# Performance work log

Hardware: AMD Instinct MI355X
Metric: run time of the kernel (lower is better)

## Reference

```python
import jax, jax.numpy as jnp
import numpy as np
from jax import lax

NUM_LAYERS, C, HIDDEN = 3, 64, 128
B, H, W = 16, 128, 128
DC = C // 4  # partial-conv channels (dim_conv = dim // 4)


def _conv2d(x, w, b=None, groups=1):
    # x: [B,C,H,W], w: [O, C//groups, kh, kw], SAME padding, stride 1
    y = lax.conv_general_dilated(x, w, (1, 1), 'SAME',
                                 dimension_numbers=('NCHW', 'OIHW', 'NCHW'),
                                 feature_group_count=groups)
    return y if b is None else y + b[None, :, None, None]


def _pw(x, w, b):
    # 1x1x1 Conv3d at T=1 == pointwise channel mix. w: [O, C], b: [O]
    return jnp.einsum('oc,bchw->bohw', w, x) + b[None, :, None, None]


def _gelu(x):
    return jax.nn.gelu(x, approximate=False)  # torch nn.GELU default (erf)


def setup_inputs() -> dict:
    key = jax.random.key(0)
    ks = jax.random.split(key, 18)
    s = 0.1
    return {
        'x': jax.random.normal(ks[0], (B, C, H, W), jnp.float32),
        'wz1': jax.random.normal(ks[1], (NUM_LAYERS, C, C), jnp.float32) * s,
        'bz1': jax.random.normal(ks[2], (NUM_LAYERS, C), jnp.float32) * s,
        'wz2': jax.random.normal(ks[3], (NUM_LAYERS, C, C), jnp.float32) * s,
        'bz2': jax.random.normal(ks[4], (NUM_LAYERS, C), jnp.float32) * s,
        'wf1': jax.random.normal(ks[5], (NUM_LAYERS, C, C), jnp.float32) * s,
        'bf1': jax.random.normal(ks[6], (NUM_LAYERS, C), jnp.float32) * s,
        'wf2': jax.random.normal(ks[7], (NUM_LAYERS, C, C), jnp.float32) * s,
        'bf2': jax.random.normal(ks[8], (NUM_LAYERS, C), jnp.float32) * s,
        # FRFN
        'pconv_w': jax.random.normal(ks[9], (NUM_LAYERS, DC, DC, 3, 3), jnp.float32) * s,
        'lin1_w': jax.random.normal(ks[10], (NUM_LAYERS, C, 2 * HIDDEN), jnp.float32) * s,
        'lin1_b': jax.random.normal(ks[11], (NUM_LAYERS, 2 * HIDDEN), jnp.float32) * s,
        'dw_w': jax.random.normal(ks[12], (NUM_LAYERS, HIDDEN, 1, 3, 3), jnp.float32) * s,
        'dw_b': jax.random.normal(ks[13], (NUM_LAYERS, HIDDEN), jnp.float32) * s,
        'lin2_w': jax.random.normal(ks[14], (NUM_LAYERS, HIDDEN, C), jnp.float32) * s,
        'lin2_b': jax.random.normal(ks[15], (NUM_LAYERS, C), jnp.float32) * s,
        # conv_out: in_dim -> out_dim=1, 3x3
        'out_w': jax.random.normal(ks[16], (1, C, 3, 3), jnp.float32) * s,
        'out_b': jax.random.normal(ks[17], (1,), jnp.float32) * s,
    }


def reference(x, wz1, bz1, wz2, bz2, wf1, bf1, wf2, bf2,
              pconv_w, lin1_w, lin1_b, dw_w, dw_b, lin2_w, lin2_b,
              out_w, out_b):
    x_init = x
    for l in range(NUM_LAYERS):
        # ---- MHRB: time dim is 1 (x.unsqueeze(2)), so flips over dim 2 are
        # identities and the recurrence is a single step h = (1 - F) * Z.
        Z = jnp.tanh(_pw(jnp.tanh(_pw(x, wz1[l], bz1[l])), wz2[l], bz2[l]))
        F = jax.nn.sigmoid(_pw(jnp.tanh(_pw(x, wf1[l], bf1[l])), wf2[l], bf2[l]))
        x = (1.0 - F) * Z
        # ---- FRFN (operates on b (h w) c; equivalently on NCHW channel dim)
        res = x
        x1 = _conv2d(x[:, :DC], pconv_w[l])            # partial 3x3 conv, no bias
        x = jnp.concatenate([x1, x[:, DC:]], axis=1)
        h = _gelu(jnp.einsum('bchw,ck->bkhw', x, lin1_w[l])
                  + lin1_b[l][None, :, None, None])    # linear1 + GELU
        h1, h2 = h[:, :HIDDEN], h[:, HIDDEN:]          # chunk(2, dim=-1)
        h1 = _gelu(_conv2d(h1, dw_w[l], dw_b[l], groups=HIDDEN))  # dwconv + GELU
        g = h1 * h2                                    # gating
        x = (jnp.einsum('bkhw,kc->bchw', g, lin2_w[l])
             + lin2_b[l][None, :, None, None]) + res   # linear2 + residual
    return _conv2d(x + x_init, out_w, out_b)           # conv_out
```

## Files before the change

kernel.cpp:

```cpp
#include <hip/hip_runtime.h>
#include <hip/hip_bf16.h>

#define CC 64
#define HIDN 128
#define DCC 16
#define HH 128
#define WW 128
#define HWS (HH*WW)
#define BB 16
#define NPIX (BB*HWS)

typedef __hip_bfloat16 bf16;
typedef __attribute__((ext_vector_type(8))) unsigned short ushort8;
typedef __attribute__((ext_vector_type(4))) unsigned short ushort4v;
typedef __attribute__((ext_vector_type(4))) float float4v;
typedef __attribute__((ext_vector_type(8))) short bf16x8;
typedef __attribute__((ext_vector_type(4))) float f32x4;

__device__ __forceinline__ float rcp_fast(float x){ return __builtin_amdgcn_rcpf(x); }
__device__ __forceinline__ float ftanh(float x){
    float e = __expf(2.f*x);
    return 1.f - 2.f*rcp_fast(e + 1.f);
}
__device__ __forceinline__ float fsig(float x){
    return rcp_fast(1.f + __expf(-x));
}
__device__ __forceinline__ float fgelu(float x){
    return x * fsig(x*(1.5957691216f + 0.07135481283f*x*x));
}
__device__ __forceinline__ float b2f(bf16 v){ return __bfloat162float(v); }
__device__ __forceinline__ float u2f(unsigned short u){
    unsigned v = ((unsigned)u) << 16; return __uint_as_float(v);
}
__device__ __forceinline__ unsigned short f2u(float f){
    bf16 h = __float2bfloat16(f);
    return *reinterpret_cast<unsigned short*>(&h);
}
__device__ __forceinline__ bf16x8 packf(float4v a, float4v b){
    bf16x8 r;
    r[0]=(short)f2u(a.x); r[1]=(short)f2u(a.y); r[2]=(short)f2u(a.z); r[3]=(short)f2u(a.w);
    r[4]=(short)f2u(b.x); r[5]=(short)f2u(b.y); r[6]=(short)f2u(b.z); r[7]=(short)f2u(b.w);
    return r;
}

template<int F32>
__global__ __launch_bounds__(256,2) void k_gate(
    const float* __restrict__ xf, const bf16* __restrict__ xb,
    const float* __restrict__ wz1, const float* __restrict__ bz1,
    const float* __restrict__ wz2, const float* __restrict__ bz2,
    const float* __restrict__ wf1, const float* __restrict__ bf1,
    const float* __restrict__ wf2, const float* __restrict__ bf2,
    bf16* __restrict__ vout)
{
    __shared__ __align__(16) unsigned short xs[512*64];
    const int t = threadIdx.x;
    const int lane = t & 63;
    const int wv = t >> 6;
    const int col = lane & 15;
    const int g = lane >> 4;
    const int blk = blockIdx.x;
    const int b = blk >> 5;
    const int sp0 = (blk & 31) << 9;

    {
        const int ch = t & 63;
        const int wg = t >> 6;
        const size_t base = ((size_t)b*CC + ch)*HWS + sp0;
        #pragma unroll
        for (int i=0;i<16;++i){
            int bufpx = (wg*16 + i) << 3;
            ushort8 val;
            if (F32){
                float4v a = *reinterpret_cast<const float4v*>(xf + base + bufpx);
                float4v c = *reinterpret_cast<const float4v*>(xf + base + bufpx + 4);
                val[0]=f2u(a.x); val[1]=f2u(a.y); val[2]=f2u(a.z); val[3]=f2u(a.w);
                val[4]=f2u(c.x); val[5]=f2u(c.y); val[6]=f2u(c.z); val[7]=f2u(c.w);
            } else {
                val = *reinterpret_cast<const ushort8*>(xb + base + bufpx);
            }
            #pragma unroll
            for (int j=0;j<8;++j){
                int px = bufpx + j;
                *(unsigned short*)((char*)xs + px*128 + ((ch*2) ^ ((px&7)<<4))) = val[j];
            }
        }
    }

    bf16x8 Az1[4][2], Af1[4][2], Az2[4][2], Af2[4][2];
    #pragma unroll
    for (int ot=0; ot<4; ++ot){
        #pragma unroll
        for (int kh=0; kh<2; ++kh){
            const float* p;
            p = wz1 + (ot*16+col)*64 + kh*32 + g*8;
            Az1[ot][kh] = packf(*(const float4v*)p, *(const float4v*)(p+4));
            p = wf1 + (ot*16+col)*64 + kh*32 + g*8;
            Af1[ot][kh] = packf(*(const float4v*)p, *(const float4v*)(p+4));
            p = wz2 + (ot*16+col)*64 + kh*32 + g*4;
            Az2[ot][kh] = packf(*(const float4v*)p, *(const float4v*)(p+16));
            p = wf2 + (ot*16+col)*64 + kh*32 + g*4;
            Af2[ot][kh] = packf(*(const float4v*)p, *(const float4v*)(p+16));
        }
    }
    __syncthreads();

    bf16* vb = vout + (size_t)b*CC*HWS;

    for (int it = wv; it < 32; it += 4){
        const int lpx = it*16 + col;
        const int px = sp0 + lpx;
        bf16x8 Bx[2];
        Bx[0] = *(const bf16x8*)((char*)xs + lpx*128 + ((g*16) ^ ((lpx&7)<<4)));
        Bx[1] = *(const bf16x8*)((char*)xs + lpx*128 + ((64 + g*16) ^ ((lpx&7)<<4)));
        f32x4 Dz[4], Df[4];
        #pragma unroll
        for (int ot=0; ot<4; ++ot){
            Dz[ot] = *(const f32x4*)(bz1 + ot*16 + g*4);
            Df[ot] = *(const f32x4*)(bf1 + ot*16 + g*4);
        }
        #pragma unroll
        for (int kh=0; kh<2; ++kh)
            #pragma unroll
            for (int ot=0; ot<4; ++ot){
                Dz[ot] = __builtin_amdgcn_mfma_f32_16x16x32_bf16(Az1[ot][kh], Bx[kh], Dz[ot], 0,0,0);
                Df[ot] = __builtin_amdgcn_mfma_f32_16x16x32_bf16(Af1[ot][kh], Bx[kh], Df[ot], 0,0,0);
            }
        #pragma unroll
        for (int ot=0; ot<4; ++ot)
            #pragma unroll
            for (int r=0; r<4; ++r){
                Dz[ot][r] = ftanh(Dz[ot][r]);
                Df[ot][r] = ftanh(Df[ot][r]);
            }
        bf16x8 Bz[2], Bf[2];
        #pragma unroll
        for (int kh=0; kh<2; ++kh)
            #pragma unroll
            for (int j=0; j<4; ++j){
                Bz[kh][j]   = (short)f2u(Dz[2*kh][j]);
                Bz[kh][4+j] = (short)f2u(Dz[2*kh+1][j]);
                Bf[kh][j]   = (short)f2u(Df[2*kh][j]);
                Bf[kh][4+j] = (short)f2u(Df[2*kh+1][j]);
            }
        f32x4 Ez[4], Ef[4];
        #pragma unroll
        for (int ot=0; ot<4; ++ot){
            Ez[ot] = *(const f32x4*)(bz2 + ot*16 + g*4);
            Ef[ot] = *(const f32x4*)(bf2 + ot*16 + g*4);
        }
        #pragma unroll
        for (int kh=0; kh<2; ++kh)
            #pragma unroll
            for (int ot=0; ot<4; ++ot){
                Ez[ot] = __builtin_amdgcn_mfma_f32_16x16x32_bf16(Az2[ot][kh], Bz[kh], Ez[ot], 0,0,0);
                Ef[ot] = __builtin_amdgcn_mfma_f32_16x16x32_bf16(Af2[ot][kh], Bf[kh], Ef[ot], 0,0,0);
            }
        #pragma unroll
        for (int ot=0; ot<4; ++ot)
            #pragma unroll
            for (int r=0; r<4; ++r){
                float Zv = ftanh(Ez[ot][r]);
                float Fv = fsig(Ef[ot][r]);
                *reinterpret_cast<unsigned short*>(vb + (size_t)(ot*16+g*4+r)*HWS + px)
                    = f2u((1.f - Fv)*Zv);
            }
    }
}

__global__ __launch_bounds__(256) void k_pconv(
    const bf16* __restrict__ v, const float* __restrict__ w, bf16* __restrict__ x1)
{
    int blk0 = blockIdx.x;
    int blk = (blk0 & 7)*32 + (blk0 >> 3);
    int gid = blk*256 + threadIdx.x;
    int b = gid >> 12;
    int sp4 = (gid & 4095) << 2;
    int y = sp4 >> 7, x0 = sp4 & 127;
    const bf16* vb = v + (size_t)b*CC*HWS;
    float acc[DCC][4];
    #pragma unroll
    for (int o=0;o<DCC;++o)
        #pragma unroll
        for (int i=0;i<4;++i) acc[o][i] = 0.f;

    #pragma unroll 1
    for (int ic=0; ic<DCC; ++ic){
        const bf16* ip = vb + (size_t)ic*HWS;
        float xv[3][6];
        #pragma unroll
        for (int ky=0;ky<3;++ky){
            int yy = y + ky - 1;
            if (yy >= 0 && yy < HH){
                const bf16* rp = ip + yy*WW + x0;
                ushort4v mv = *reinterpret_cast<const ushort4v*>(rp);
                xv[ky][1]=u2f(mv[0]); xv[ky][2]=u2f(mv[1]);
                xv[ky][3]=u2f(mv[2]); xv[ky][4]=u2f(mv[3]);
                xv[ky][0] = (x0>0)     ? b2f(rp[-1]) : 0.f;
                xv[ky][5] = (x0+4<WW)  ? b2f(rp[4])  : 0.f;
            } else {
                #pragma unroll
                for (int i=0;i<6;++i) xv[ky][i] = 0.f;
            }
        }
        #pragma unroll
        for (int o=0;o<DCC;++o){
            const float* wp = w + (size_t)(o*DCC+ic)*9;
            #pragma unroll
            for (int ky=0;ky<3;++ky){
                float w0 = wp[ky*3+0], w1 = wp[ky*3+1], w2 = wp[ky*3+2];
                #pragma unroll
                for (int i=0;i<4;++i)
                    acc[o][i] = fmaf(w0, xv[ky][i],
                                fmaf(w1, xv[ky][i+1],
                                fmaf(w2, xv[ky][i+2], acc[o][i])));
            }
        }
    }
    bf16* xo = x1 + (size_t)b*DCC*HWS + sp4;
    #pragma unroll
    for (int o=0;o<DCC;++o){
        ushort4v ov;
        #pragma unroll
        for (int i=0;i<4;++i) ov[i] = f2u(acc[o][i]);
        *reinterpret_cast<ushort4v*>(xo + (size_t)o*HWS) = ov;
    }
}

__global__ __launch_bounds__(256) void k_lin1h(
    const bf16* __restrict__ x1, const bf16* __restrict__ v,
    const float* __restrict__ l1w, const float* __restrict__ l1b,
    bf16* __restrict__ h1out)
{
    __shared__ __align__(16) unsigned short xs[256*64];
    __shared__ __align__(16) unsigned short tr[4][32*66];
    const int t = threadIdx.x;
    const int lane = t & 63;
    const int wv = t >> 6;
    const int col = lane & 15;
    const int g = lane >> 4;
    const int blk = blockIdx.x;
    const int b = blk >> 6;
    const int sp0 = (blk & 63) << 8;

    {
        const int ch = t & 63;
        const int wg = t >> 6;
        const bf16* src = (ch < DCC) ? x1 + ((size_t)b*DCC + ch)*HWS
                                     : v  + ((size_t)b*CC  + ch)*HWS;
        #pragma unroll
        for (int i=0;i<8;++i){
            int bufpx = (wg*8 + i) << 3;
            ushort8 val = *reinterpret_cast<const ushort8*>(src + sp0 + bufpx);
            #pragma unroll
            for (int j=0;j<8;++j){
                int px = bufpx + j;
                *(unsigned short*)((char*)xs + px*128 + ((ch*2) ^ ((px&7)<<4))) = val[j];
            }
        }
    }
    __syncthreads();

    unsigned short* trw = &tr[wv][0];
    const int lpx0 = wv*64;

    #pragma unroll 1
    for (int oc=0; oc<4; ++oc){
        bf16x8 A1[2][2];
        #pragma unroll
        for (int t2=0;t2<2;++t2)
            #pragma unroll
            for (int kh=0;kh<2;++kh){
                bf16x8 fa;
                #pragma unroll
                for (int j=0;j<8;++j){
                    int cin = kh*32 + g*8 + j;
                    fa[j] = (short)f2u(l1w[cin*256 + oc*32 + t2*16 + col]);
                }
                A1[t2][kh]=fa;
            }
        #pragma unroll
        for (int lt=0;lt<4;++lt){
            int px = lpx0 + lt*16 + col;
            bf16x8 B0 = *(const bf16x8*)((char*)xs + px*128 + ((g*16) ^ ((px&7)<<4)));
            bf16x8 B1 = *(const bf16x8*)((char*)xs + px*128 + ((64 + g*16) ^ ((px&7)<<4)));
            f32x4 D0 = *(const f32x4*)(l1b + oc*32 + g*4);
            f32x4 D1 = *(const f32x4*)(l1b + oc*32 + 16 + g*4);
            D0 = __builtin_amdgcn_mfma_f32_16x16x32_bf16(A1[0][0], B0, D0, 0,0,0);
            D0 = __builtin_amdgcn_mfma_f32_16x16x32_bf16(A1[0][1], B1, D0, 0,0,0);
            D1 = __builtin_amdgcn_mfma_f32_16x16x32_bf16(A1[1][0], B0, D1, 0,0,0);
            D1 = __builtin_amdgcn_mfma_f32_16x16x32_bf16(A1[1][1], B1, D1, 0,0,0);
            int lp = lt*16 + col;
            #pragma unroll
            for (int rr=0;rr<4;++rr){
                trw[(g*4+rr)*66 + lp]    = f2u(fgelu(D0[rr]));
                trw[(16+g*4+rr)*66 + lp] = f2u(fgelu(D1[rr]));
            }
        }
        {
            int ch2 = lane >> 1;
            int half = lane & 1;
            const unsigned short* srcp = trw + ch2*66 + half*32;
            bf16* dst = h1out + ((size_t)(b*HIDN + oc*32 + ch2))*HWS + sp0 + lpx0 + half*32;
            #pragma unroll
            for (int i=0;i<4;++i){
                ushort8 u8 = *reinterpret_cast<const ushort8*>(srcp + i*8);
                *reinterpret_cast<ushort8*>(dst + i*8) = u8;
            }
        }
    }
}

__global__ __launch_bounds__(256) void k_wprep(
    const float* __restrict__ l1w_all, const float* __restrict__ w2_all,
    bf16* __restrict__ frag_all)
{
    const int l = blockIdx.x;
    const float* l1w = l1w_all + (size_t)l*CC*256;
    const float* w2  = w2_all  + (size_t)l*HIDN*CC;
    unsigned short* buf1 = (unsigned short*)(frag_all + (size_t)l*16384);
    unsigned short* buf2 = buf1 + 8192;
    const int t = threadIdx.x;
    const int lane = t & 63;
    const int col = lane & 15;
    const int g = lane >> 4;
    #pragma unroll
    for (int c4=0;c4<4;++c4){
        int combo = (t>>6)*4 + c4;
        {
            int cc = combo >> 2, t2 = (combo>>1)&1, kh = combo&1;
            #pragma unroll
            for (int j=0;j<8;++j){
                int cin = kh*32 + g*8 + j;
                buf1[(combo*64 + lane)*8 + j] =
                    f2u(l1w[cin*256 + 128 + cc*32 + t2*16 + col]);
            }
        }
        {
            int cc = combo >> 2, ot = combo & 3;
            #pragma unroll
            for (int j=0;j<8;++j){
                int k = cc*32 + ((j>>2)<<4) + (g<<2) + (j&3);
                buf2[(combo*64 + lane)*8 + j] = f2u(w2[k*64 + ot*16 + col]);
            }
        }
    }
}

__global__ __launch_bounds__(256) void k_dwA(
    const bf16* __restrict__ x1, const bf16* __restrict__ v,
    const bf16* __restrict__ h1, const bf16* __restrict__ wfrag,
    const float* __restrict__ l1b,
    const float* __restrict__ dww, const float* __restrict__ dwb,
    const float* __restrict__ l2b,
    bf16* __restrict__ xout,
    const float* __restrict__ xinit,
    bf16* __restrict__ xsum)
{
    __shared__ __align__(16) unsigned short xs[128*64];
    __shared__ __align__(16) unsigned short ubuf[2*8320];
    const int t = threadIdx.x;
    const int lane = t & 63;
    const int wv = t >> 6;
    const int col = lane & 15;
    const int g = lane >> 4;
    const int blk0 = blockIdx.x;
    const int blk = (blk0 & 7)*256 + (blk0 >> 3);
    const int b = blk >> 7;
    const int y = blk & 127;

    const int cj  = (t>>3) & 31;
    const int pxo = (t & 7) << 4;

    const unsigned short* buf1 = (const unsigned short*)wfrag;
    const unsigned short* buf2 = buf1 + 8192;

    ushort8 pfa[3], pfb[3];
    unsigned short pfl[3], pfr[3];
    float pw9[9], pbj;
    auto LOADCHUNK = [&](int cc){
        int chg = cc*32 + cj;
        const bf16* h1p = h1 + ((size_t)(b*HIDN + chg))*HWS;
        #pragma unroll
        for (int ky=0; ky<3; ++ky){
            int gy = y + ky - 1;
            if (gy >= 0 && gy < HH){
                const bf16* rp = h1p + (size_t)gy*WW + pxo;
                pfa[ky] = *reinterpret_cast<const ushort8*>(rp);
                pfb[ky] = *reinterpret_cast<const ushort8*>(rp+8);
                pfl[ky] = (pxo>0)     ? *reinterpret_cast<const unsigned short*>(rp-1)  : 0;
                pfr[ky] = (pxo+16<WW) ? *reinterpret_cast<const unsigned short*>(rp+16) : 0;
            } else {
                #pragma unroll
                for (int i=0;i<8;++i){ pfa[ky][i]=0; pfb[ky][i]=0; }
                pfl[ky]=0; pfr[ky]=0;
            }
        }
        #pragma unroll
        for (int i=0;i<9;++i) pw9[i] = dww[chg*9+i];
        pbj = dwb[chg];
    };

    LOADCHUNK(0);

    {
        const int ch = t & 63;
        const int wg = t >> 6;
        const bf16* src = (ch < DCC) ? x1 + ((size_t)b*DCC + ch)*HWS
                                     : v  + ((size_t)b*CC  + ch)*HWS;
        #pragma unroll
        for (int i=0;i<2;++i){
            int bufpx = (wg*2 + i) << 3;
            ushort8 val = *reinterpret_cast<const ushort8*>(src + (size_t)y*WW + bufpx);
            #pragma unroll
            for (int j=0;j<8;++j){
                int px = bufpx + j;
                *(unsigned short*)((char*)xs + px*128 + ((ch*2) ^ ((px&7)<<4))) = val[j];
            }
        }
    }
    __syncthreads();

    f32x4 Dx[2][4];
    #pragma unroll
    for (int q=0;q<2;++q)
        #pragma unroll
        for (int ot=0;ot<4;++ot)
            Dx[q][ot] = *(const f32x4*)(l2b + ot*16 + g*4);

    #pragma unroll 1
    for (int cc=0; cc<4; ++cc){
        unsigned short* ub = ubuf + (cc&1)*8320;
        ushort8 o0v, o1v;
        {
            float acc[16];
            #pragma unroll
            for (int i=0;i<16;++i) acc[i]=0.f;
            #pragma unroll
            for (int ky=0; ky<3; ++ky){
                float m[16];
                #pragma unroll
                for (int i=0;i<8;++i){ m[i]=u2f(pfa[ky][i]); m[8+i]=u2f(pfb[ky][i]); }
                float lf = u2f(pfl[ky]);
                float rt = u2f(pfr[ky]);
                float w0=pw9[ky*3], w1=pw9[ky*3+1], wv2=pw9[ky*3+2];
                #pragma unroll
                for (int i=0;i<16;++i){
                    float l  = i ? m[i-1] : lf;
                    float r_ = (i==15) ? rt : m[i+1];
                    acc[i] = fmaf(w0,l, fmaf(w1,m[i], fmaf(wv2,r_,acc[i])));
                }
            }
            #pragma unroll
            for (int i=0;i<8;++i){
                o0v[i] = f2u(fgelu(acc[i]+pbj));
                o1v[i] = f2u(fgelu(acc[8+i]+pbj));
            }
        }
        if (cc < 3) LOADCHUNK(cc+1);
        *(ushort8*)(ub + cj*260 + pxo)     = o0v;
        *(ushort8*)(ub + cj*260 + pxo + 8) = o1v;
        __syncthreads();
        {
            bf16x8 A1g[2][2];
            #pragma unroll
            for (int t2=0;t2<2;++t2)
                #pragma unroll
                for (int kh=0;kh<2;++kh){
                    int combo = (cc*2+t2)*2+kh;
                    ushort8 u = *reinterpret_cast<const ushort8*>(buf1 + (combo*64 + lane)*8);
                    bf16x8 f;
                    #pragma unroll
                    for (int j=0;j<8;++j) f[j]=(short)u[j];
                    A1g[t2][kh]=f;
                }
            bf16x8 A2[4];
            #pragma unroll
            for (int ot=0;ot<4;++ot){
                int combo = cc*4+ot;
                ushort8 u = *reinterpret_cast<const ushort8*>(buf2 + (combo*64 + lane)*8);
                bf16x8 f;
                #pragma unroll
                for (int j=0;j<8;++j) f[j]=(short)u[j];
                A2[ot] = f;
            }
            #pragma unroll
            for (int q=0;q<2;++q){
                int px = (wv*2+q)*16 + col;
                bf16x8 B0 = *(const bf16x8*)((char*)xs + px*128 + ((g*16) ^ ((px&7)<<4)));
                bf16x8 B1 = *(const bf16x8*)((char*)xs + px*128 + ((64 + g*16) ^ ((px&7)<<4)));
                f32x4 D0 = *(const f32x4*)(l1b + 128 + cc*32 + g*4);
                f32x4 D1 = *(const f32x4*)(l1b + 128 + cc*32 + 16 + g*4);
                D0 = __builtin_amdgcn_mfma_f32_16x16x32_bf16(A1g[0][0], B0, D0, 0,0,0);
                D0 = __builtin_amdgcn_mfma_f32_16x16x32_bf16(A1g[0][1], B1, D0, 0,0,0);
                D1 = __builtin_amdgcn_mfma_f32_16x16x32_bf16(A1g[1][0], B0, D1, 0,0,0);
                D1 = __builtin_amdgcn_mfma_f32_16x16x32_bf16(A1g[1][1], B1, D1, 0,0,0);
                bf16x8 Bg;
                #pragma unroll
                for (int j=0;j<4;++j){
                    float u0 = u2f(ub[(g*4+j)*260 + px]);
                    float u1 = u2f(ub[(16+g*4+j)*260 + px]);
                    Bg[j]   = (short)f2u(u0 * fgelu(D0[j]));
                    Bg[4+j] = (short)f2u(u1 * fgelu(D1[j]));
                }
                #pragma unroll
                for (int ot=0;ot<4;++ot)
                    Dx[q][ot] = __builtin_amdgcn_mfma_f32_16x16x32_bf16(A2[ot], Bg, Dx[q][ot], 0,0,0);
            }
        }
    }
    __syncthreads();
    #pragma unroll
    for (int q=0;q<2;++q)
        #pragma unroll
        for (int ot=0;ot<4;++ot)
            #pragma unroll
            for (int rr=0;rr<4;++rr)
                ubuf[(ot*16 + g*4 + rr)*136 + (wv*2+q)*16 + col] = f2u(Dx[q][ot][rr]);
    __syncthreads();
    {
        int ch  = t >> 2;
        int pxb = (t & 3) * 32;
        size_t off = ((size_t)(b*CC + ch))*HWS + (size_t)y*WW + pxb;
        #pragma unroll
        for (int i=0;i<4;++i){
            ushort8 dv = *reinterpret_cast<const ushort8*>(ubuf + ch*136 + pxb + i*8);
            ushort8 vv = *reinterpret_cast<const ushort8*>(v + off + i*8);
            ushort8 ov;
            float rv[8];
            #pragma unroll
            for (int j=0;j<8;++j){
                rv[j] = u2f(dv[j]) + u2f(vv[j]);
                ov[j] = f2u(rv[j]);
            }
            *reinterpret_cast<ushort8*>(xout + off + i*8) = ov;
            if (xinit){
                float4v x0 = *reinterpret_cast<const float4v*>(xinit + off + i*8);
                float4v x1v = *reinterpret_cast<const float4v*>(xinit + off + i*8 + 4);
                ushort8 sv;
                sv[0]=f2u(rv[0]+x0.x); sv[1]=f2u(rv[1]+x0.y);
                sv[2]=f2u(rv[2]+x0.z); sv[3]=f2u(rv[3]+x0.w);
                sv[4]=f2u(rv[4]+x1v.x); sv[5]=f2u(rv[5]+x1v.y);
                sv[6]=f2u(rv[6]+x1v.z); sv[7]=f2u(rv[7]+x1v.w);
                *reinterpret_cast<ushort8*>(xsum + off + i*8) = sv;
            }
        }
    }
}

__global__ __launch_bounds__(256) void k_final(
    const bf16* __restrict__ s, const float* __restrict__ w,
    const float* __restrict__ bias, float* __restrict__ out)
{
    int gid = blockIdx.x*256 + threadIdx.x;
    int b = gid >> 12;
    int sp4 = (gid & 4095) << 2;
    int y = sp4 >> 7, x0 = sp4 & 127;
    const bf16* sb = s + (size_t)b*CC*HWS;
    float acc[4];
    #pragma unroll
    for (int i=0;i<4;++i) acc[i] = bias[0];

    #pragma unroll 1
    for (int c=0;c<CC;++c){
        const bf16* ip = sb + (size_t)c*HWS;
        const float* wp = w + (size_t)c*9;
        #pragma unroll
        for (int ky=0;ky<3;++ky){
            int yy = y + ky - 1;
            float xv[6];
            if (yy >= 0 && yy < HH){
                const bf16* rp = ip + yy*WW + x0;
                ushort4v mv = *reinterpret_cast<const ushort4v*>(rp);
                xv[1]=u2f(mv[0]); xv[2]=u2f(mv[1]); xv[3]=u2f(mv[2]); xv[4]=u2f(mv[3]);
                xv[0] = (x0>0)    ? b2f(rp[-1]) : 0.f;
                xv[5] = (x0+4<WW) ? b2f(rp[4])  : 0.f;
            } else {
                #pragma unroll
                for (int i=0;i<6;++i) xv[i] = 0.f;
            }
            float w0 = wp[ky*3+0], w1 = wp[ky*3+1], w2 = wp[ky*3+2];
            #pragma unroll
            for (int i=0;i<4;++i)
                acc[i] = fmaf(w0, xv[i],
                         fmaf(w1, xv[i+1],
                         fmaf(w2, xv[i+2], acc[i])));
        }
    }
    float4v ov; ov.x=acc[0]; ov.y=acc[1]; ov.z=acc[2]; ov.w=acc[3];
    *reinterpret_cast<float4v*>(out + (size_t)gid*4) = ov;
}

extern "C" void kernel_launch(void* const* d_in, const int* in_sizes, int n_in,
                              void* d_out, int out_size, void* d_ws, size_t ws_size,
                              hipStream_t stream)
{
    const float* x    = (const float*)d_in[0];
    const float* wz1  = (const float*)d_in[1];
    const float* bz1  = (const float*)d_in[2];
    const float* wz2  = (const float*)d_in[3];
    const float* bz2  = (const float*)d_in[4];
    const float* wf1  = (const float*)d_in[5];
    const float* bf1  = (const float*)d_in[6];
    const float* wf2  = (const float*)d_in[7];
    const float* bf2  = (const float*)d_in[8];
    const float* pw   = (const float*)d_in[9];
    const float* l1w  = (const float*)d_in[10];
    const float* l1b  = (const float*)d_in[11];
    const float* dww  = (const float*)d_in[12];
    const float* dwb  = (const float*)d_in[13];
    const float* l2w  = (const float*)d_in[14];
    const float* l2b  = (const float*)d_in[15];
    const float* ow   = (const float*)d_in[16];
    const float* obb  = (const float*)d_in[17];

    char* ws = (char*)d_ws;
    bf16* xc    = (bf16*)(ws);
    bf16* v     = (bf16*)(ws + 33554432);
    bf16* x1    = (bf16*)(ws + 67108864);
    bf16* xsumb = (bf16*)(ws + 75497472);
    bf16* h1buf = (bf16*)(ws + 109051904);
    bf16* wfrag = (bf16*)(ws + 176160768);

    k_wprep<<<3, 256, 0, stream>>>(l1w, l2w, wfrag);
    for (int l=0;l<3;++l){
        if (l == 0)
            k_gate<1><<<512, 256, 0, stream>>>(x, nullptr,
                wz1 + l*CC*CC, bz1 + l*CC, wz2 + l*CC*CC, bz2 + l*CC,
                wf1 + l*CC*CC, bf1 + l*CC, wf2 + l*CC*CC, bf2 + l*CC, v);
        else
            k_gate<0><<<512, 256, 0, stream>>>(nullptr, xc,
                wz1 + l*CC*CC, bz1 + l*CC, wz2 + l*CC*CC, bz2 + l*CC,
                wf1 + l*CC*CC, bf1 + l*CC, wf2 + l*CC*CC, bf2 + l*CC, v);
        k_pconv<<<NPIX/(256*4), 256, 0, stream>>>(v, pw + l*DCC*DCC*9, x1);
        k_lin1h<<<NPIX/256, 256, 0, stream>>>(x1, v,
                l1w + l*CC*256, l1b + l*256, h1buf);
        k_dwA  <<<BB*HH, 256, 0, stream>>>(x1, v, h1buf, wfrag + (size_t)l*16384,
                l1b + l*256,
                dww + l*HIDN*9, dwb + l*HIDN,
                l2b + l*CC,
                xc, (l==2) ? x : nullptr, xsumb);
    }
    k_final<<<NPIX/(256*4), 256, 0, stream>>>(xsumb, ow, obb, (float*)d_out);
}
```

Measured before the change: 729.5 us.

## Fuse partial 3x3 conv into lin1 kernel using shared-memory halo rows

Removes the standalone k_pconv kernel. Each k_pl1 block now covers two image rows, loads the 16 partial-conv channels plus one halo row above and below into shared memory, computes the 3x3 conv there, and writes the result both into the swizzled lin1 input tile and to global x1, which the later dw kernel still reads. This saves one launch and the round trip of x1 through global memory before lin1. In exchange each block does the conv work inside the lin1 kernel, uses more shared memory (which may lower occupancy), and rereads the halo rows.

```diff
diff --git a/kernel.cpp b/kernel.cpp
--- a/kernel.cpp
+++ b/kernel.cpp
@@ -167,71 +167,13 @@
     }
 }
 
-__global__ __launch_bounds__(256) void k_pconv(
-    const bf16* __restrict__ v, const float* __restrict__ w, bf16* __restrict__ x1)
-{
-    int blk0 = blockIdx.x;
-    int blk = (blk0 & 7)*32 + (blk0 >> 3);
-    int gid = blk*256 + threadIdx.x;
-    int b = gid >> 12;
-    int sp4 = (gid & 4095) << 2;
-    int y = sp4 >> 7, x0 = sp4 & 127;
-    const bf16* vb = v + (size_t)b*CC*HWS;
-    float acc[DCC][4];
-    #pragma unroll
-    for (int o=0;o<DCC;++o)
-        #pragma unroll
-        for (int i=0;i<4;++i) acc[o][i] = 0.f;
-
-    #pragma unroll 1
-    for (int ic=0; ic<DCC; ++ic){
-        const bf16* ip = vb + (size_t)ic*HWS;
-        float xv[3][6];
-        #pragma unroll
-        for (int ky=0;ky<3;++ky){
-            int yy = y + ky - 1;
-            if (yy >= 0 && yy < HH){
-                const bf16* rp = ip + yy*WW + x0;
-                ushort4v mv = *reinterpret_cast<const ushort4v*>(rp);
-                xv[ky][1]=u2f(mv[0]); xv[ky][2]=u2f(mv[1]);
-                xv[ky][3]=u2f(mv[2]); xv[ky][4]=u2f(mv[3]);
-                xv[ky][0] = (x0>0)     ? b2f(rp[-1]) : 0.f;
-                xv[ky][5] = (x0+4<WW)  ? b2f(rp[4])  : 0.f;
-            } else {
-                #pragma unroll
-                for (int i=0;i<6;++i) xv[ky][i] = 0.f;
-            }
-        }
-        #pragma unroll
-        for (int o=0;o<DCC;++o){
-            const float* wp = w + (size_t)(o*DCC+ic)*9;
-            #pragma unroll
-            for (int ky=0;ky<3;++ky){
-                float w0 = wp[ky*3+0], w1 = wp[ky*3+1], w2 = wp[ky*3+2];
-                #pragma unroll
-                for (int i=0;i<4;++i)
-                    acc[o][i] = fmaf(w0, xv[ky][i],
-                                fmaf(w1, xv[ky][i+1],
-                                fmaf(w2, xv[ky][i+2], acc[o][i])));
-            }
-        }
-    }
-    bf16* xo = x1 + (size_t)b*DCC*HWS + sp4;
-    #pragma unroll
-    for (int o=0;o<DCC;++o){
-        ushort4v ov;
-        #pragma unroll
-        for (int i=0;i<4;++i) ov[i] = f2u(acc[o][i]);
-        *reinterpret_cast<ushort4v*>(xo + (size_t)o*HWS) = ov;
-    }
-}
-
-__global__ __launch_bounds__(256) void k_lin1h(
-    const bf16* __restrict__ x1, const bf16* __restrict__ v,
+__global__ __launch_bounds__(256) void k_pl1(
+    const bf16* __restrict__ v, const float* __restrict__ pw,
     const float* __restrict__ l1w, const float* __restrict__ l1b,
-    bf16* __restrict__ h1out)
+    bf16* __restrict__ x1out, bf16* __restrict__ h1out)
 {
     __shared__ __align__(16) unsigned short xs[256*64];
+    __shared__ __align__(16) unsigned short vh[16][4][128];
     __shared__ __align__(16) unsigned short tr[4][32*66];
     const int t = threadIdx.x;
     const int lane = t & 63;
@@ -240,22 +182,91 @@
     const int g = lane >> 4;
     const int blk = blockIdx.x;
     const int b = blk >> 6;
-    const int sp0 = (blk & 63) << 8;
+    const int y0 = (blk & 63) << 1;
+    const int sp0 = y0 * WW;
 
     {
         const int ch = t & 63;
         const int wg = t >> 6;
-        const bf16* src = (ch < DCC) ? x1 + ((size_t)b*DCC + ch)*HWS
-                                     : v  + ((size_t)b*CC  + ch)*HWS;
-        #pragma unroll
-        for (int i=0;i<8;++i){
-            int bufpx = (wg*8 + i) << 3;
-            ushort8 val = *reinterpret_cast<const ushort8*>(src + sp0 + bufpx);
-            #pragma unroll
-            for (int j=0;j<8;++j){
-                int px = bufpx + j;
-                *(unsigned short*)((char*)xs + px*128 + ((ch*2) ^ ((px&7)<<4))) = val[j];
-            }
+        if (ch < DCC){
+            int gy = y0 - 1 + wg;
+            unsigned short* dst = &vh[ch][wg][0];
+            if (gy >= 0 && gy < HH){
+                const bf16* src = v + ((size_t)b*CC + ch)*HWS + (size_t)gy*WW;
+                #pragma unroll
+                for (int i=0;i<16;++i)
+                    *reinterpret_cast<ushort8*>(dst + i*8) =
+                        *reinterpret_cast<const ushort8*>(src + i*8);
+            } else {
+                #pragma unroll
+                for (int i=0;i<16;++i){
+                    ushort8 z; 
+                    #pragma unroll
+                    for (int j=0;j<8;++j) z[j]=0;
+                    *reinterpret_cast<ushort8*>(dst + i*8) = z;
+                }
+            }
+        } else {
+            const bf16* src = v + ((size_t)b*CC + ch)*HWS + sp0;
+            #pragma unroll
+            for (int i=0;i<8;++i){
+                int bufpx = wg*64 + i*8;
+                ushort8 val = *reinterpret_cast<const ushort8*>(src + bufpx);
+                #pragma unroll
+                for (int j=0;j<8;++j){
+                    int px = bufpx + j;
+                    *(unsigned short*)((char*)xs + px*128 + ((ch*2) ^ ((px&7)<<4))) = val[j];
+                }
+            }
+        }
+    }
+    __syncthreads();
+
+    {
+        const int oc = t >> 4;
+        const int px0 = (t & 15) << 3;
+        float acc[2][8];
+        #pragma unroll
+        for (int r=0;r<2;++r)
+            #pragma unroll
+            for (int i=0;i<8;++i) acc[r][i]=0.f;
+        #pragma unroll 1
+        for (int ic=0; ic<DCC; ++ic){
+            float m[4][10];
+            #pragma unroll
+            for (int row=0;row<4;++row){
+                const unsigned short* rp = &vh[ic][row][px0];
+                ushort8 mv = *reinterpret_cast<const ushort8*>(rp);
+                #pragma unroll
+                for (int i=0;i<8;++i) m[row][i+1] = u2f(mv[i]);
+                m[row][0] = (px0>0)    ? u2f(rp[-1]) : 0.f;
+                m[row][9] = (px0+8<WW) ? u2f(rp[8])  : 0.f;
+            }
+            const float* wp = pw + (size_t)(oc*DCC+ic)*9;
+            #pragma unroll
+            for (int ky=0;ky<3;++ky){
+                float w0 = wp[ky*3+0], w1 = wp[ky*3+1], w2 = wp[ky*3+2];
+                #pragma unroll
+                for (int r=0;r<2;++r)
+                    #pragma unroll
+                    for (int i=0;i<8;++i)
+                        acc[r][i] = fmaf(w0, m[r+ky][i],
+                                    fmaf(w1, m[r+ky][i+1],
+                                    fmaf(w2, m[r+ky][i+2], acc[r][i])));
+            }
+        }
+        #pragma unroll
+        for (int r=0;r<2;++r){
+            ushort8 ov;
+            #pragma unroll
+            for (int i=0;i<8;++i){
+                unsigned short uu = f2u(acc[r][i]);
+                ov[i] = uu;
+                int px = r*128 + px0 + i;
+                *(unsigned short*)((char*)xs + px*128 + ((oc*2) ^ ((px&7)<<4))) = uu;
+            }
+            *reinterpret_cast<ushort8*>(x1out + ((size_t)b*DCC + oc)*HWS
+                                        + (size_t)(y0+r)*WW + px0) = ov;
         }
     }
     __syncthreads();
@@ -631,9 +642,8 @@
             k_gate<0><<<512, 256, 0, stream>>>(nullptr, xc,
                 wz1 + l*CC*CC, bz1 + l*CC, wz2 + l*CC*CC, bz2 + l*CC,
                 wf1 + l*CC*CC, bf1 + l*CC, wf2 + l*CC*CC, bf2 + l*CC, v);
-        k_pconv<<<NPIX/(256*4), 256, 0, stream>>>(v, pw + l*DCC*DCC*9, x1);
-        k_lin1h<<<NPIX/256, 256, 0, stream>>>(x1, v,
-                l1w + l*CC*256, l1b + l*256, h1buf);
+        k_pl1  <<<NPIX/256, 256, 0, stream>>>(v, pw + l*DCC*DCC*9,
+                l1w + l*CC*256, l1b + l*256, x1, h1buf);
         k_dwA  <<<BB*HH, 256, 0, stream>>>(x1, v, h1buf, wfrag + (size_t)l*16384,
                 l1b + l*256,
                 dww + l*HIDN*9, dwb + l*HIDN,
```

Result: faster. 668.1 us (-8.4%).
